# Kernel tuning notes

Measured on AMD Instinct MI355X. Metric: run time of the kernel, lower is better.

Reference implementation:

```python
import jax, jax.numpy as jnp
import numpy as np

B, S, NX, NH = 2, 2048, 1024, 16
HD = NX // NH  # head dim = 64


def setup_inputs() -> dict:
    key = jax.random.key(0)
    k1, k2, k3 = jax.random.split(key, 3)
    x = jax.random.normal(k1, (B, S, NX), dtype=jnp.float32)
    w_attn = jax.random.normal(k2, (NX, 3 * NX), dtype=jnp.float32) * 0.02
    b_attn = jnp.zeros((3 * NX,), dtype=jnp.float32)
    w_proj = jax.random.normal(k3, (NX, NX), dtype=jnp.float32) * 0.02
    b_proj = jnp.zeros((NX,), dtype=jnp.float32)
    return {"x": x, "w_attn": w_attn, "b_attn": b_attn, "w_proj": w_proj, "b_proj": b_proj}


def _split_heads(t):
    # [B, S, NX] -> [B, NH, S, HD]
    b, s, _ = t.shape
    return t.reshape(b, s, NH, HD).transpose(0, 2, 1, 3)


def reference(x, w_attn, b_attn, w_proj, b_proj):
    # c_attn: Conv1D == affine projection to fused QKV
    qkv = jnp.einsum("bsi,io->bso", x, w_attn) + b_attn  # [B, S, 3*NX]
    q, k, v = jnp.split(qkv, 3, axis=2)
    q, k, v = _split_heads(q), _split_heads(k), _split_heads(v)  # [B, NH, S, HD]

    # scaled dot-product scores (scale=True)
    w = jnp.einsum("bhqd,bhkd->bhqk", q, k) / jnp.sqrt(jnp.asarray(HD, dtype=q.dtype))

    # causal mask via multiply-subtract (matches TF: w*b - 10000*(1-b))
    nd = ns = S
    i = jnp.arange(nd)[:, None]
    j = jnp.arange(ns)[None, :]
    b = (i >= j - ns + nd).astype(w.dtype)  # [nd, ns]
    w = w * b - 10000.0 * (1.0 - b)

    w = jax.nn.softmax(w, axis=-1)  # stable_softmax
    # attn_dropout / head_mask: identity (inference, no head mask)

    a = jnp.einsum("bhqk,bhkd->bhqd", w, v)  # [B, NH, S, HD]
    # merge heads -> [B, S, NX]
    a = a.transpose(0, 2, 1, 3).reshape(B, S, NX)
    # c_proj
    out = jnp.einsum("bsi,io->bso", a, w_proj) + b_proj
    return out
```

## Files before the change

### kernel.cpp

```cpp
#include <hip/hip_runtime.h>
#include <stdint.h>

typedef __attribute__((ext_vector_type(8))) short short8;
typedef __attribute__((ext_vector_type(4))) float f32x4;
typedef __attribute__((ext_vector_type(16))) float f32x16;
typedef __attribute__((ext_vector_type(4))) unsigned short ushort4v;
typedef __attribute__((ext_vector_type(2))) int int2v;

#define BB 2
#define SS 2048
#define NXDIM 1024
#define NHEADS 16
#define HDIM 64

__device__ __forceinline__ unsigned short f2bf(float f){
  unsigned int u = __float_as_uint(f);
  u += 0x7fffu + ((u >> 16) & 1u);
  return (unsigned short)(u >> 16);
}

__device__ __forceinline__ void gload_lds16(const void* g, void* l){
  __builtin_amdgcn_global_load_lds((const __attribute__((address_space(1))) void*)g,
                                   (__attribute__((address_space(3))) void*)l, 16, 0, 0);
}

__device__ __forceinline__ unsigned cvt_pk_bf16(float lo, float hi){
  unsigned r;
  asm("v_cvt_pk_bf16_f32 %0, %1, %2" : "=v"(r) : "v"(lo), "v"(hi));
  return r;
}

__device__ __forceinline__ int2v ds_tr_b16(unsigned addr){
  int2v r;
  asm volatile("ds_read_b64_tr_b16 %0, %1" : "=v"(r) : "v"(addr));
  return r;
}

__device__ __forceinline__ int2v plswap(int a, int b){
  return __builtin_amdgcn_permlane32_swap(a, b, false, false);
}
__device__ __forceinline__ float plmax(float x){
  int2v r = plswap(__float_as_int(x), __float_as_int(x));
  return fmaxf(__int_as_float(r.x), __int_as_float(r.y));
}
__device__ __forceinline__ float pladd(float x){
  int2v r = plswap(__float_as_int(x), __float_as_int(x));
  return __int_as_float(r.x) + __int_as_float(r.y);
}

__global__ __launch_bounds__(256) void f32_to_bf16_k(const float* __restrict__ in,
                                                     unsigned short* __restrict__ out, int n4){
  int i = blockIdx.x * 256 + threadIdx.x;
  if (i >= n4) return;
  float4 v = ((const float4*)in)[i];
  ushort4v r = { f2bf(v.x), f2bf(v.y), f2bf(v.z), f2bf(v.w) };
  ((ushort4v*)out)[i] = r;
}

__global__ __launch_bounds__(256) void transpose_bf16_k(const float* __restrict__ in,
                                                        unsigned short* __restrict__ out,
                                                        int R, int C){
  __shared__ float t[32][33];
  const int bx = blockIdx.x * 32, by = blockIdx.y * 32;
  const int tx = threadIdx.x, ty = threadIdx.y;
  #pragma unroll
  for (int i = ty; i < 32; i += 8)
    t[i][tx] = in[(size_t)(by + i) * C + bx + tx];
  __syncthreads();
  #pragma unroll
  for (int i = ty; i < 32; i += 8)
    out[(size_t)(bx + i) * R + by + tx] = f2bf(t[tx][i]);
}

template<bool OUT_F32>
__global__ __launch_bounds__(256) void gemm_bt_k(const unsigned short* __restrict__ A,
                                                 const unsigned short* __restrict__ BT,
                                                 const float* __restrict__ bias,
                                                 void* __restrict__ Cout,
                                                 int M, int N, int K)
{
  __shared__ unsigned short As[128*32];
  __shared__ unsigned short Bs[128*32];
  const int tid = threadIdx.x;
  const int w = tid >> 6, lane = tid & 63;
  const int l15 = lane & 15, g = lane >> 4;
  const int wr = w >> 1, wc = w & 1;
  const int m0 = blockIdx.y * 128, n0 = blockIdx.x * 128;

  f32x4 acc[4][4];
  #pragma unroll
  for (int m=0;m<4;m++)
    #pragma unroll
    for (int n=0;n<4;n++) acc[m][n] = (f32x4){0.f,0.f,0.f,0.f};

  const int scol = (lane & 3) * 8;

  for (int k0 = 0; k0 < K; k0 += 32){
    __syncthreads();
    #pragma unroll
    for (int j=0;j<2;j++){
      const int row = w*32 + j*16 + (lane >> 2);
      const unsigned short* ga = A  + (size_t)(m0 + row) * K + (k0 + scol);
      const unsigned short* gb = BT + (size_t)(n0 + row) * K + (k0 + scol);
      gload_lds16(ga, &As[(w*32 + j*16) * 32]);
      gload_lds16(gb, &Bs[(w*32 + j*16) * 32]);
    }
    __syncthreads();

    short8 af[4], bf[4];
    #pragma unroll
    for (int m=0;m<4;m++) af[m] = *(const short8*)&As[(wr*64 + m*16 + l15)*32 + g*8];
    #pragma unroll
    for (int n=0;n<4;n++) bf[n] = *(const short8*)&Bs[(wc*64 + n*16 + l15)*32 + g*8];
    #pragma unroll
    for (int m=0;m<4;m++)
      #pragma unroll
      for (int n=0;n<4;n++)
        acc[m][n] = __builtin_amdgcn_mfma_f32_16x16x32_bf16(af[m], bf[n], acc[m][n], 0, 0, 0);
  }

  const int crow0 = m0 + wr*64;
  const int ccol0 = n0 + wc*64;
  #pragma unroll
  for (int n=0;n<4;n++){
    const int col = ccol0 + n*16 + l15;
    const float bv = bias[col];
    #pragma unroll
    for (int m=0;m<4;m++){
      #pragma unroll
      for (int r=0;r<4;r++){
        const int row = crow0 + m*16 + g*4 + r;
        const float v = acc[m][n][r] + bv;
        if (OUT_F32) ((float*)Cout)[(size_t)row * N + col] = v;
        else         ((unsigned short*)Cout)[(size_t)row * N + col] = f2bf(v);
      }
    }
  }
}

__global__ __launch_bounds__(512) void gemm256_k(const unsigned short* __restrict__ A,
                                                 const unsigned short* __restrict__ BT,
                                                 const float* __restrict__ bias,
                                                 unsigned short* __restrict__ Cout,
                                                 int M, int N, int K)
{
  __shared__ unsigned short As[2][256*64];
  __shared__ unsigned short Bs[2][192*64];
  const int tid = threadIdx.x;
  const int w = tid >> 6, lane = tid & 63;
  const int l15 = lane & 15, g = lane >> 4;
  const int wm = w >> 2, wn = w & 3;
  const int m0 = blockIdx.y * 256, n0 = blockIdx.x * 192;

  f32x4 acc[8][3];
  #pragma unroll
  for (int m=0;m<8;m++)
    #pragma unroll
    for (int n=0;n<3;n++) acc[m][n] = (f32x4){0.f,0.f,0.f,0.f};

  const int srow = lane >> 3;
  const int scol = 8 * ((lane & 7) ^ (lane >> 3));

  auto stageA = [&](int bi, int k0, int j){
    const int r = w*32 + j*8 + srow;
    gload_lds16(A + (size_t)(m0 + r) * K + (k0 + scol), &As[bi][(w*32 + j*8)*64]);
  };
  auto stageB = [&](int bi, int k0, int j){
    const int r = w*24 + j*8 + srow;
    gload_lds16(BT + (size_t)(n0 + r) * K + (k0 + scol), &Bs[bi][(w*24 + j*8)*64]);
  };

  #pragma unroll
  for (int j=0;j<4;j++) stageA(0, 0, j);
  #pragma unroll
  for (int j=0;j<3;j++) stageB(0, 0, j);
  asm volatile("s_waitcnt vmcnt(0)" ::: "memory");
  __syncthreads();

  const int niter = K >> 6;
  int cur = 0;

  for (int t = 0; t < niter; ++t){
    const int k1 = (t+1) << 6;
    const bool pref = (t+1) < niter;
    const char* Ab = (const char*)&As[cur][0];
    const char* Bb = (const char*)&Bs[cur][0];

    short8 bf[3][2];
    #pragma unroll
    for (int nf=0;nf<3;nf++){
      const int row = wn*48 + nf*16 + l15;
      #pragma unroll
      for (int kk=0;kk<2;kk++)
        bf[nf][kk] = *(const short8*)(Bb + row*128 + ((kk*64 + g*16) ^ ((l15&7)<<4)));
    }

    #pragma unroll
    for (int ph=0; ph<4; ++ph){
      if (pref){ stageA(cur^1, k1, ph); if (ph < 3) stageB(cur^1, k1, ph); }

      short8 af[2][2];
      #pragma unroll
      for (int i=0;i<2;i++){
        const int mf = ph*2 + i;
        const int row = wm*128 + mf*16 + l15;
        #pragma unroll
        for (int kk=0;kk<2;kk++)
          af[i][kk] = *(const short8*)(Ab + row*128 + ((kk*64 + g*16) ^ ((l15&7)<<4)));
      }
      asm volatile("s_waitcnt lgkmcnt(0)" ::: "memory");
      __builtin_amdgcn_sched_barrier(0);

      __builtin_amdgcn_s_setprio(1);
      #pragma unroll
      for (int i=0;i<2;i++)
        #pragma unroll
        for (int nf=0;nf<3;nf++)
          #pragma unroll
          for (int kk=0;kk<2;kk++)
            acc[ph*2+i][nf] = __builtin_amdgcn_mfma_f32_16x16x32_bf16(af[i][kk], bf[nf][kk],
                                                                      acc[ph*2+i][nf], 0, 0, 0);
      __builtin_amdgcn_s_setprio(0);
    }

    asm volatile("s_waitcnt vmcnt(0)" ::: "memory");
    __syncthreads();
    cur ^= 1;
  }

  const int crow0 = m0 + wm*128;
  const int ccol0 = n0 + wn*48;
  #pragma unroll
  for (int nf=0;nf<3;nf++){
    const int col = ccol0 + nf*16 + l15;
    const float bv = bias[col];
    #pragma unroll
    for (int mf=0;mf<8;mf++){
      #pragma unroll
      for (int r=0;r<4;r++){
        const int row = crow0 + mf*16 + g*4 + r;
        Cout[(size_t)row * N + col] = f2bf(acc[mf][nf][r] + bv);
      }
    }
  }
}

__global__ __launch_bounds__(512) void attn_k(const unsigned short* __restrict__ qkv,
                                              unsigned short* __restrict__ aout)
{
  const int xy = ((int)blockIdx.x + (int)blockIdx.y) & 15;
  const int qb = blockIdx.z ? xy : (15 - xy);
  const int h = blockIdx.y, b = blockIdx.z;
  const int tid = threadIdx.x;
  const int w = tid >> 6, lane = tid & 63;
  const int l31 = lane & 31, hi = lane >> 5;
  const int qw = w >> 1, p = w & 1;

  __shared__ unsigned short lds[32768];
  unsigned short* Ksb = lds;
  unsigned short* Vsb = lds + 16384;

  const size_t rs = 3 * NXDIM;
  const unsigned short* Qg = qkv + (size_t)b * SS * rs + h * HDIM;
  const unsigned short* Kg = Qg + NXDIM;
  const unsigned short* Vg = Qg + 2 * NXDIM;

  const int q0w = qb*128 + qw*32;
  const int q   = q0w + l31;
  const int qw_hi = q0w + 31;

  short8 qf[4];
  #pragma unroll
  for (int c=0;c<4;c++)
    qf[c] = *(const short8*)(Qg + (size_t)q * rs + c*16 + 8*hi);

  f32x16 O0, O1;
  #pragma unroll
  for (int r=0;r<16;r++){ O0[r]=0.f; O1[r]=0.f; }
  float m_run = -1e30f, l_run = 0.f;
  const float SC2 = 0.125f * 1.44269504089f;
  const float THRR = 44.36f;

  const int krow_in = lane >> 3;
  const int kcol    = 8 * ((lane & 7) ^ (lane >> 3));
  const int v_d     = ((lane >> 3) & 3) * 16 + 8 * (lane & 1);
  const unsigned vtr_base = (unsigned)(size_t)Vsb + 8u*(unsigned)lane + 768u*(unsigned)hi;

  auto stage = [&](int bi, int tt){
    unsigned short* Kd = Ksb + (p*2 + bi)*4096;
    unsigned short* Vd = Vsb + (p*2 + bi)*4096;
    #pragma unroll
    for (int j=0;j<2;j++){
      const int ch = qw*2 + j;
      const int krow = tt*64 + ch*8 + krow_in;
      gload_lds16(Kg + (size_t)krow * rs + kcol, Kd + ch*512);
      const int vkv = tt*64 + (ch*2 + hi)*4 + ((lane>>1)&3);
      gload_lds16(Vg + (size_t)vkv * rs + v_d, Vd + ch*512);
    }
  };

  const int tmax = 2*qb + 1;
  stage(0, p);
  __syncthreads();
  int cur = 0;

  for (int t = p; t <= tmax; t += 2){
    if (t + 2 <= tmax) stage(cur^1, t+2);

    const char* Kb = (const char*)(Ksb + (p*2 + cur)*4096);
    const unsigned vb = vtr_base + (unsigned)((p*2 + cur)*8192);

    #pragma unroll
    for (int kvs=0;kvs<2;kvs++){
      const int kv_lo = t*64 + kvs*32;
      if (kv_lo > qw_hi) continue;

      f32x16 S;
      #pragma unroll
      for (int r=0;r<16;r++) S[r] = 0.f;
      __builtin_amdgcn_s_setprio(1);
      #pragma unroll
      for (int c=0;c<4;c++){
        const int row = kvs*32 + l31;
        short8 kf = *(const short8*)(Kb + row*128 + ((c*32 + 16*hi) ^ ((row&7)<<4)));
        S = __builtin_amdgcn_mfma_f32_32x32x16_bf16(kf, qf[c], S, 0, 0, 0);
      }
      __builtin_amdgcn_s_setprio(0);

      int2v tv[8];
      #pragma unroll
      for (int c=0;c<2;c++)
        #pragma unroll
        for (int dh=0;dh<2;dh++)
          #pragma unroll
          for (int eb=0;eb<2;eb++)
            tv[c*4+dh*2+eb] = ds_tr_b16(vb + (unsigned)((kvs*8 + c*4 + eb)*512 + dh*256));

      float mA=-1e30f, mB=-1e30f, mC=-1e30f, mD=-1e30f;
      if (kv_lo + 31 > q0w){
        #pragma unroll
        for (int r=0;r<16;r+=4){
          const int kvb = kv_lo + 8*(r>>2) + 4*hi;
          float s0 = (kvb+0 <= q) ? S[r+0] : -1e30f;
          float s1 = (kvb+1 <= q) ? S[r+1] : -1e30f;
          float s2 = (kvb+2 <= q) ? S[r+2] : -1e30f;
          float s3 = (kvb+3 <= q) ? S[r+3] : -1e30f;
          S[r+0]=s0; S[r+1]=s1; S[r+2]=s2; S[r+3]=s3;
          mA = fmaxf(mA, s0); mB = fmaxf(mB, s1); mC = fmaxf(mC, s2); mD = fmaxf(mD, s3);
        }
      } else {
        #pragma unroll
        for (int r=0;r<16;r+=4){
          mA = fmaxf(mA, S[r+0]); mB = fmaxf(mB, S[r+1]);
          mC = fmaxf(mC, S[r+2]); mD = fmaxf(mD, S[r+3]);
        }
      }
      float mx = fmaxf(fmaxf(mA,mB), fmaxf(mC,mD));
      mx = plmax(mx);

      if (!__all(mx <= m_run + THRR)){
        const float m_new = fmaxf(m_run, mx);
        const float corr = __builtin_exp2f((m_run - m_new) * SC2);
        m_run = m_new;
        l_run *= corr;
        #pragma unroll
        for (int r=0;r<16;r++){ O0[r] *= corr; O1[r] *= corr; }
      }
      const float msc = m_run * SC2;

      float lA=0.f, lB=0.f, lC=0.f, lD=0.f;
      #pragma unroll
      for (int r=0;r<16;r+=4){
        float p0=__builtin_exp2f(__builtin_fmaf(S[r+0],SC2,-msc));
        float p1=__builtin_exp2f(__builtin_fmaf(S[r+1],SC2,-msc));
        float p2=__builtin_exp2f(__builtin_fmaf(S[r+2],SC2,-msc));
        float p3=__builtin_exp2f(__builtin_fmaf(S[r+3],SC2,-msc));
        S[r+0]=p0; S[r+1]=p1; S[r+2]=p2; S[r+3]=p3;
        lA+=p0; lB+=p1; lC+=p2; lD+=p3;
      }
      float ls = (lA+lB) + (lC+lD);
      ls = pladd(ls);
      l_run += ls;

      unsigned pk[8];
      #pragma unroll
      for (int i=0;i<8;i++) pk[i] = cvt_pk_bf16(S[2*i], S[2*i+1]);
      short8 pfrag[2];
      #pragma unroll
      for (int c=0;c<2;c++){
        int2v r0 = plswap((int)pk[4*c+0], (int)pk[4*c+2]);
        int2v r1 = plswap((int)pk[4*c+1], (int)pk[4*c+3]);
        union { unsigned u[4]; short8 s; } pw;
        pw.u[0] = (unsigned)r0.x; pw.u[1] = (unsigned)r1.x;
        pw.u[2] = (unsigned)r0.y; pw.u[3] = (unsigned)r1.y;
        pfrag[c] = pw.s;
      }

      asm volatile("s_waitcnt lgkmcnt(0)" ::: "memory");
      __builtin_amdgcn_sched_barrier(0);

      __builtin_amdgcn_s_setprio(1);
      #pragma unroll
      for (int c=0;c<2;c++){
        union { int2v t[2]; short8 s; } v0, v1;
        v0.t[0] = tv[c*4+0]; v0.t[1] = tv[c*4+1];
        v1.t[0] = tv[c*4+2]; v1.t[1] = tv[c*4+3];
        O0 = __builtin_amdgcn_mfma_f32_32x32x16_bf16(v0.s, pfrag[c], O0, 0, 0, 0);
        O1 = __builtin_amdgcn_mfma_f32_32x32x16_bf16(v1.s, pfrag[c], O1, 0, 0, 0);
      }
      __builtin_amdgcn_s_setprio(0);
    }

    __syncthreads();
    cur ^= 1;
  }

  float* sm = (float*)lds + qw * (64*34);
  if (p){
    #pragma unroll
    for (int r=0;r<16;r++){ sm[lane*34 + r] = O0[r]; sm[lane*34 + 16 + r] = O1[r]; }
    sm[lane*34 + 32] = m_run;
    sm[lane*34 + 33] = l_run;
  }
  __syncthreads();
  if (!p){
    const float m1 = sm[lane*34 + 32], l1 = sm[lane*34 + 33];
    const float mm = fmaxf(m_run, m1);
    const float c0 = __builtin_exp2f((m_run - mm) * SC2);
    const float c1 = __builtin_exp2f((m1 - mm) * SC2);
    const float inv = 1.f / (l_run*c0 + l1*c1);
    unsigned short* dst = aout + ((size_t)b*SS + q) * NXDIM + h*HDIM;
    #pragma unroll
    for (int g4=0; g4<4; g4++){
      ushort4v a0, a1;
      #pragma unroll
      for (int i=0;i<4;i++){
        a0[i] = f2bf((O0[4*g4+i]*c0 + sm[lane*34 + 4*g4+i]*c1) * inv);
        a1[i] = f2bf((O1[4*g4+i]*c0 + sm[lane*34 + 16 + 4*g4+i]*c1) * inv);
      }
      *(ushort4v*)(dst + 8*g4 + 4*hi)      = a0;
      *(ushort4v*)(dst + 32 + 8*g4 + 4*hi) = a1;
    }
  }
}

extern "C" void kernel_launch(void* const* d_in, const int* in_sizes, int n_in,
                              void* d_out, int out_size, void* d_ws, size_t ws_size,
                              hipStream_t stream){
  (void)in_sizes; (void)n_in; (void)out_size; (void)ws_size;
  const float* x      = (const float*)d_in[0];
  const float* w_attn = (const float*)d_in[1];
  const float* b_attn = (const float*)d_in[2];
  const float* w_proj = (const float*)d_in[3];
  const float* b_proj = (const float*)d_in[4];
  float* out = (float*)d_out;

  unsigned short* xb   = (unsigned short*)d_ws;
  unsigned short* waT  = xb  + (size_t)4096*1024;
  unsigned short* wpT  = waT + (size_t)3072*1024;
  unsigned short* qkv  = wpT + (size_t)1024*1024;
  unsigned short* aout = qkv + (size_t)4096*3072;

  f32_to_bf16_k<<<4096, 256, 0, stream>>>(x, xb, 4096*1024/4);
  transpose_bf16_k<<<dim3(3072/32, 1024/32), dim3(32,8), 0, stream>>>(w_attn, waT, 1024, 3072);
  transpose_bf16_k<<<dim3(1024/32, 1024/32), dim3(32,8), 0, stream>>>(w_proj, wpT, 1024, 1024);

  gemm256_k<<<dim3(3072/192, 4096/256), 512, 0, stream>>>(xb, waT, b_attn, qkv, 4096, 3072, 1024);
  attn_k<<<dim3(SS/128, NHEADS, BB), 512, 0, stream>>>(qkv, aout);
  gemm_bt_k<true><<<dim3(1024/128, 4096/128), 256, 0, stream>>>(aout, wpT, b_proj, (void*)out, 4096, 1024, 1024);
}
```

Before: 119.1 us.

## Shrink output-projection GEMM tiles, hoist QKV prefetch, stage QKV epilogue through LDS

The output projection GEMM now uses 64x64 tiles instead of 128x128, giving 1024 blocks rather than 256 so more of the CUs are busy, at the cost of less data reuse per block. The QKV GEMM issues all next-tile prefetch loads at the start of each iteration instead of spreading them across the four compute phases. Its epilogue now writes bf16 results into LDS and then stores them to global memory as coalesced 16-byte rows, replacing the scattered 2-byte stores.

```diff
diff --git a/kernel.cpp b/kernel.cpp
--- a/kernel.cpp
+++ b/kernel.cpp
@@ -72,67 +72,59 @@
     out[(size_t)(bx + i) * R + by + tx] = f2bf(t[tx][i]);
 }
 
-template<bool OUT_F32>
-__global__ __launch_bounds__(256) void gemm_bt_k(const unsigned short* __restrict__ A,
-                                                 const unsigned short* __restrict__ BT,
-                                                 const float* __restrict__ bias,
-                                                 void* __restrict__ Cout,
-                                                 int M, int N, int K)
+__global__ __launch_bounds__(256) void gemm2_64_k(const unsigned short* __restrict__ A,
+                                                  const unsigned short* __restrict__ BT,
+                                                  const float* __restrict__ bias,
+                                                  float* __restrict__ Cout,
+                                                  int M, int N, int K)
 {
-  __shared__ unsigned short As[128*32];
-  __shared__ unsigned short Bs[128*32];
+  __shared__ unsigned short As[64*32];
+  __shared__ unsigned short Bs[64*32];
   const int tid = threadIdx.x;
   const int w = tid >> 6, lane = tid & 63;
   const int l15 = lane & 15, g = lane >> 4;
   const int wr = w >> 1, wc = w & 1;
-  const int m0 = blockIdx.y * 128, n0 = blockIdx.x * 128;
-
-  f32x4 acc[4][4];
-  #pragma unroll
-  for (int m=0;m<4;m++)
-    #pragma unroll
-    for (int n=0;n<4;n++) acc[m][n] = (f32x4){0.f,0.f,0.f,0.f};
-
+  const int m0 = blockIdx.y * 64, n0 = blockIdx.x * 64;
+
+  f32x4 acc[2][2];
+  #pragma unroll
+  for (int m=0;m<2;m++)
+    #pragma unroll
+    for (int n=0;n<2;n++) acc[m][n] = (f32x4){0.f,0.f,0.f,0.f};
+
+  const int srow_in = lane >> 2;
   const int scol = (lane & 3) * 8;
 
   for (int k0 = 0; k0 < K; k0 += 32){
     __syncthreads();
-    #pragma unroll
-    for (int j=0;j<2;j++){
-      const int row = w*32 + j*16 + (lane >> 2);
-      const unsigned short* ga = A  + (size_t)(m0 + row) * K + (k0 + scol);
-      const unsigned short* gb = BT + (size_t)(n0 + row) * K + (k0 + scol);
-      gload_lds16(ga, &As[(w*32 + j*16) * 32]);
-      gload_lds16(gb, &Bs[(w*32 + j*16) * 32]);
-    }
+    gload_lds16(A  + (size_t)(m0 + w*16 + srow_in) * K + (k0 + scol), &As[(w*16)*32]);
+    gload_lds16(BT + (size_t)(n0 + w*16 + srow_in) * K + (k0 + scol), &Bs[(w*16)*32]);
     __syncthreads();
 
-    short8 af[4], bf[4];
-    #pragma unroll
-    for (int m=0;m<4;m++) af[m] = *(const short8*)&As[(wr*64 + m*16 + l15)*32 + g*8];
-    #pragma unroll
-    for (int n=0;n<4;n++) bf[n] = *(const short8*)&Bs[(wc*64 + n*16 + l15)*32 + g*8];
-    #pragma unroll
-    for (int m=0;m<4;m++)
-      #pragma unroll
-      for (int n=0;n<4;n++)
+    short8 af[2], bf[2];
+    #pragma unroll
+    for (int m=0;m<2;m++) af[m] = *(const short8*)&As[(wr*32 + m*16 + l15)*32 + g*8];
+    #pragma unroll
+    for (int n=0;n<2;n++) bf[n] = *(const short8*)&Bs[(wc*32 + n*16 + l15)*32 + g*8];
+    #pragma unroll
+    for (int m=0;m<2;m++)
+      #pragma unroll
+      for (int n=0;n<2;n++)
         acc[m][n] = __builtin_amdgcn_mfma_f32_16x16x32_bf16(af[m], bf[n], acc[m][n], 0, 0, 0);
   }
 
-  const int crow0 = m0 + wr*64;
-  const int ccol0 = n0 + wc*64;
-  #pragma unroll
-  for (int n=0;n<4;n++){
+  const int crow0 = m0 + wr*32;
+  const int ccol0 = n0 + wc*32;
+  #pragma unroll
+  for (int n=0;n<2;n++){
     const int col = ccol0 + n*16 + l15;
     const float bv = bias[col];
     #pragma unroll
-    for (int m=0;m<4;m++){
+    for (int m=0;m<2;m++){
       #pragma unroll
       for (int r=0;r<4;r++){
         const int row = crow0 + m*16 + g*4 + r;
-        const float v = acc[m][n][r] + bv;
-        if (OUT_F32) ((float*)Cout)[(size_t)row * N + col] = v;
-        else         ((unsigned short*)Cout)[(size_t)row * N + col] = f2bf(v);
+        Cout[(size_t)row * N + col] = acc[m][n][r] + bv;
       }
     }
   }
@@ -144,8 +136,9 @@
                                                  unsigned short* __restrict__ Cout,
                                                  int M, int N, int K)
 {
-  __shared__ unsigned short As[2][256*64];
-  __shared__ unsigned short Bs[2][192*64];
+  __shared__ unsigned short lds[57344];
+  unsigned short* As0 = lds;
+  unsigned short* Bs0 = lds + 32768;
   const int tid = threadIdx.x;
   const int w = tid >> 6, lane = tid & 63;
   const int l15 = lane & 15, g = lane >> 4;
@@ -163,11 +156,11 @@
 
   auto stageA = [&](int bi, int k0, int j){
     const int r = w*32 + j*8 + srow;
-    gload_lds16(A + (size_t)(m0 + r) * K + (k0 + scol), &As[bi][(w*32 + j*8)*64]);
+    gload_lds16(A + (size_t)(m0 + r) * K + (k0 + scol), As0 + bi*16384 + (w*32 + j*8)*64);
   };
   auto stageB = [&](int bi, int k0, int j){
     const int r = w*24 + j*8 + srow;
-    gload_lds16(BT + (size_t)(n0 + r) * K + (k0 + scol), &Bs[bi][(w*24 + j*8)*64]);
+    gload_lds16(BT + (size_t)(n0 + r) * K + (k0 + scol), Bs0 + bi*12288 + (w*24 + j*8)*64);
   };
 
   #pragma unroll
@@ -182,9 +175,15 @@
 
   for (int t = 0; t < niter; ++t){
     const int k1 = (t+1) << 6;
-    const bool pref = (t+1) < niter;
-    const char* Ab = (const char*)&As[cur][0];
-    const char* Bb = (const char*)&Bs[cur][0];
+    if (t+1 < niter){
+      #pragma unroll
+      for (int j=0;j<4;j++) stageA(cur^1, k1, j);
+      #pragma unroll
+      for (int j=0;j<3;j++) stageB(cur^1, k1, j);
+    }
+
+    const char* Ab = (const char*)(As0 + cur*16384);
+    const char* Bb = (const char*)(Bs0 + cur*12288);
 
     short8 bf[3][2];
     #pragma unroll
@@ -197,8 +196,6 @@
 
     #pragma unroll
     for (int ph=0; ph<4; ++ph){
-      if (pref){ stageA(cur^1, k1, ph); if (ph < 3) stageB(cur^1, k1, ph); }
-
       short8 af[2][2];
       #pragma unroll
       for (int i=0;i<2;i++){
@@ -228,20 +225,24 @@
     cur ^= 1;
   }
 
-  const int crow0 = m0 + wm*128;
-  const int ccol0 = n0 + wn*48;
+  unsigned short* ct = lds;
   #pragma unroll
   for (int nf=0;nf<3;nf++){
-    const int col = ccol0 + nf*16 + l15;
-    const float bv = bias[col];
+    const int col = wn*48 + nf*16 + l15;
+    const float bv = bias[n0 + col];
     #pragma unroll
     for (int mf=0;mf<8;mf++){
       #pragma unroll
-      for (int r=0;r<4;r++){
-        const int row = crow0 + mf*16 + g*4 + r;
-        Cout[(size_t)row * N + col] = f2bf(acc[mf][nf][r] + bv);
-      }
-    }
+      for (int r=0;r<4;r++)
+        ct[(wm*128 + mf*16 + g*4 + r)*192 + col] = f2bf(acc[mf][nf][r] + bv);
+    }
+  }
+  __syncthreads();
+  #pragma unroll
+  for (int u = 0; u < 12; ++u){
+    const int idx = u*512 + tid;
+    const int row = idx / 24, sl = idx % 24;
+    *(short8*)(Cout + (size_t)(m0 + row) * N + n0 + sl*8) = *(const short8*)&ct[row*192 + sl*8];
   }
 }
 
@@ -467,5 +468,5 @@
 
   gemm256_k<<<dim3(3072/192, 4096/256), 512, 0, stream>>>(xb, waT, b_attn, qkv, 4096, 3072, 1024);
   attn_k<<<dim3(SS/128, NHEADS, BB), 512, 0, stream>>>(qkv, aout);
-  gemm_bt_k<true><<<dim3(1024/128, 4096/128), 256, 0, stream>>>(aout, wpT, b_proj, (void*)out, 4096, 1024, 1024);
-}
+  gemm2_64_k<<<dim3(1024/64, 4096/64), 256, 0, stream>>>(aout, wpT, b_proj, out, 4096, 1024, 1024);
+}
```

Measured after the change: 113.4 us. -4.7%, faster.
